# Kernel tuning notes

Measured on AMD Instinct MI355X. Metric: run time of the kernel, lower is better.

## Reference

```python
import jax, jax.numpy as jnp
import numpy as np

B, H, W = 8, 64, 64
DIM_RGB, DIM_PL, EMBED, OUT = 256, 256, 128, 256
BN_EPS = 1e-5


def conv1x1(x, w, b=None):
    # x: (B,C,H,W), w: (D,C) -> (B,D,H,W)
    y = jnp.einsum('bchw,dc->bdhw', x, w)
    if b is not None:
        y = y + b[None, :, None, None]
    return y


def spatial_attention(q, k, v, scale):
    # q,k,v: (B,D,H,W)
    b, d, h, w = q.shape
    n = h * w
    qf = q.reshape(b, d, n).transpose(0, 2, 1)   # (B,N,D)
    kf = k.reshape(b, d, n)                       # (B,D,N)
    vf = v.reshape(b, d, n).transpose(0, 2, 1)   # (B,N,D)
    attn = jax.nn.softmax(jnp.einsum('bnd,bdm->bnm', qf, kf) * scale, axis=-1)
    out = jnp.einsum('bnm,bmd->bnd', attn, vf)   # (B,N,D)
    return out.transpose(0, 2, 1).reshape(b, d, h, w)


def setup_inputs() -> dict:
    key = jax.random.key(0)
    ks = jax.random.split(key, 20)
    s = 0.05
    inp = {
        'f_rgb': jax.random.normal(ks[0], (B, DIM_RGB, H, W), jnp.float32),
        'f_pl': jax.random.normal(ks[1], (B, DIM_PL, H, W), jnp.float32),
        'w_q_rgb': jax.random.normal(ks[2], (EMBED, DIM_RGB), jnp.float32) * s,
        'b_q_rgb': jax.random.normal(ks[3], (EMBED,), jnp.float32) * s,
        'w_k_pl': jax.random.normal(ks[4], (EMBED, DIM_PL), jnp.float32) * s,
        'b_k_pl': jax.random.normal(ks[5], (EMBED,), jnp.float32) * s,
        'w_v_pl': jax.random.normal(ks[6], (EMBED, DIM_PL), jnp.float32) * s,
        'b_v_pl': jax.random.normal(ks[7], (EMBED,), jnp.float32) * s,
        'w_q_pl': jax.random.normal(ks[8], (EMBED, DIM_PL), jnp.float32) * s,
        'b_q_pl': jax.random.normal(ks[9], (EMBED,), jnp.float32) * s,
        'w_k_rgb': jax.random.normal(ks[10], (EMBED, DIM_RGB), jnp.float32) * s,
        'b_k_rgb': jax.random.normal(ks[11], (EMBED,), jnp.float32) * s,
        'w_v_rgb': jax.random.normal(ks[12], (EMBED, DIM_RGB), jnp.float32) * s,
        'b_v_rgb': jax.random.normal(ks[13], (EMBED,), jnp.float32) * s,
        'w_proj': jax.random.normal(ks[14], (OUT, 2 * EMBED), jnp.float32) * s,
        'bn_gamma': jnp.ones((OUT,), jnp.float32),
        'bn_beta': jnp.zeros((OUT,), jnp.float32),
        'bn_mean': jax.random.normal(ks[15], (OUT,), jnp.float32) * 0.01,
        'bn_var': jax.random.uniform(ks[16], (OUT,), jnp.float32, 0.5, 1.5),
    }
    return inp


def reference(f_rgb, f_pl, w_q_rgb, b_q_rgb, w_k_pl, b_k_pl, w_v_pl, b_v_pl,
              w_q_pl, b_q_pl, w_k_rgb, b_k_rgb, w_v_rgb, b_v_rgb,
              w_proj, bn_gamma, bn_beta, bn_mean, bn_var):
    scale = EMBED ** -0.5
    out_rgb2pl = spatial_attention(
        conv1x1(f_rgb, w_q_rgb, b_q_rgb),
        conv1x1(f_pl, w_k_pl, b_k_pl),
        conv1x1(f_pl, w_v_pl, b_v_pl), scale)
    out_pl2rgb = spatial_attention(
        conv1x1(f_pl, w_q_pl, b_q_pl),
        conv1x1(f_rgb, w_k_rgb, b_k_rgb),
        conv1x1(f_rgb, w_v_rgb, b_v_rgb), scale)
    combined = jnp.concatenate([out_rgb2pl, out_pl2rgb], axis=1)  # (B,2E,H,W)
    y = conv1x1(combined, w_proj)  # no bias
    # BatchNorm2d (inference form) + ReLU
    inv = bn_gamma * jax.lax.rsqrt(bn_var + BN_EPS)
    y = y * inv[None, :, None, None] + (bn_beta - bn_mean * inv)[None, :, None, None]
    return jax.nn.relu(y)
```

## Files before the change

### kernel.cpp

```cpp
#include <hip/hip_runtime.h>
#include <hip/hip_bf16.h>
#include <hip/hip_fp16.h>

typedef _Float16 f16;
typedef _Float16 f16x8 __attribute__((ext_vector_type(8)));
typedef _Float16 f16x4 __attribute__((ext_vector_type(4)));
typedef float f32x4 __attribute__((ext_vector_type(4)));

#define NP   4096
#define NB   8
#define CINC 256
#define EMB  128
#define OUTC 256
#define BN_EPS 1e-5f

#define DSZ  ((size_t)NB * NP * EMB)
#define TSZ  (2 * DSZ)

__global__ __launch_bounds__(256) void proj_all_kernel(
    const float* __restrict__ Xrgb, const float* __restrict__ Xpl,
    const float* __restrict__ w0, const float* __restrict__ b0,
    const float* __restrict__ w1, const float* __restrict__ b1,
    const float* __restrict__ w2, const float* __restrict__ b2,
    const float* __restrict__ w3, const float* __restrict__ b3,
    const float* __restrict__ w4, const float* __restrict__ b4,
    const float* __restrict__ w5, const float* __restrict__ b5,
    f16* __restrict__ Qt, f16* __restrict__ Kt, f16* __restrict__ Vn)
{
    const int m0 = blockIdx.x * 128;
    const int p  = blockIdx.y;
    const int b  = blockIdx.z;
    const int s  = (p >= 3) ? 1 : 0;
    const int j  = p - s * 3;
    const int tid = threadIdx.x;
    const int w = tid >> 6, lane = tid & 63, quad = lane >> 4, lr = lane & 15;

    const float* X  = s ? Xpl : Xrgb;
    const float* W  = p == 0 ? w0 : p == 1 ? w1 : p == 2 ? w2
                    : p == 3 ? w3 : p == 4 ? w4 : w5;
    const float* Bi = p == 0 ? b0 : p == 1 ? b1 : p == 2 ? b2
                    : p == 3 ? b3 : p == 4 ? b4 : b5;

    __shared__ __align__(16) f16 smem[128 * 72 * 2];
    f16* Al = smem;
    f16* Bl = smem + 128 * 72;

    f32x4 acc[2][8];
    #pragma unroll
    for (int mi = 0; mi < 2; ++mi)
        #pragma unroll
        for (int ni = 0; ni < 8; ++ni) acc[mi][ni] = (f32x4){0.f, 0.f, 0.f, 0.f};

    for (int kt = 0; kt < 4; ++kt) {
        const int kc0 = kt * 64;
        __syncthreads();
        for (int s2 = tid; s2 < 1024; s2 += 256) {
            const int n = s2 & 127, cg = s2 >> 7;
            f16 tmp[8];
            #pragma unroll
            for (int jj = 0; jj < 8; ++jj)
                tmp[jj] = (f16)X[((size_t)b * CINC + kc0 + cg * 8 + jj) * NP + m0 + n];
            *(f16x8*)&Al[n * 72 + cg * 8] = *(const f16x8*)tmp;
        }
        for (int s2 = tid; s2 < 1024; s2 += 256) {
            const int d = s2 >> 3, cg = s2 & 7;
            f16 tmp[8];
            #pragma unroll
            for (int jj = 0; jj < 8; ++jj)
                tmp[jj] = (f16)W[(size_t)d * CINC + kc0 + cg * 8 + jj];
            *(f16x8*)&Bl[d * 72 + cg * 8] = *(const f16x8*)tmp;
        }
        __syncthreads();
        #pragma unroll
        for (int ks = 0; ks < 2; ++ks) {
            f16x8 af[2], bfr[8];
            #pragma unroll
            for (int mi = 0; mi < 2; ++mi)
                af[mi] = *(const f16x8*)&Al[(w * 32 + mi * 16 + lr) * 72 + ks * 32 + quad * 8];
            #pragma unroll
            for (int ni = 0; ni < 8; ++ni)
                bfr[ni] = *(const f16x8*)&Bl[(ni * 16 + lr) * 72 + ks * 32 + quad * 8];
            #pragma unroll
            for (int mi = 0; mi < 2; ++mi)
                #pragma unroll
                for (int ni = 0; ni < 8; ++ni)
                    acc[mi][ni] = __builtin_amdgcn_mfma_f32_16x16x32_f16(
                        af[mi], bfr[ni], acc[mi][ni], 0, 0, 0);
        }
    }

    float bias[8];
    #pragma unroll
    for (int ni = 0; ni < 8; ++ni) bias[ni] = Bi[ni * 16 + lr];

    if (j < 2) {
        f16* out = (j == 0) ? (Qt + (size_t)s * DSZ) : (Kt + (size_t)(1 - s) * DSZ);
        #pragma unroll
        for (int mi = 0; mi < 2; ++mi)
            #pragma unroll
            for (int ni = 0; ni < 8; ++ni)
                #pragma unroll
                for (int r = 0; r < 4; ++r) {
                    const int n = m0 + w * 32 + mi * 16 + quad * 4 + r;
                    out[((size_t)b * NP + n) * EMB + ni * 16 + lr] =
                        (f16)(acc[mi][ni][r] + bias[ni]);
                }
    } else {
        f16* outV = Vn + (size_t)(1 - s) * DSZ;
        __syncthreads();
        f16* T = smem;
        #pragma unroll
        for (int mi = 0; mi < 2; ++mi)
            #pragma unroll
            for (int ni = 0; ni < 8; ++ni)
                #pragma unroll
                for (int r = 0; r < 4; ++r)
                    T[(ni * 16 + lr) * 136 + w * 32 + mi * 16 + quad * 4 + r] =
                        (f16)(acc[mi][ni][r] + bias[ni]);
        __syncthreads();
        for (int s2 = tid; s2 < 2048; s2 += 256) {
            const int d = s2 >> 4, n8 = (s2 & 15) * 8;
            *(f16x8*)&outV[((size_t)b * EMB + d) * NP + m0 + n8] =
                *(const f16x8*)&T[d * 136 + n8];
        }
    }
}

__global__ __launch_bounds__(256, 2) void attn_kernel(
    const f16* __restrict__ Qt, const f16* __restrict__ Kt,
    const f16* __restrict__ Vn, f16* __restrict__ combT)
{
    const int bid = blockIdx.x;
    const int g = bid & 15, dir = g >> 3, b = g & 7;
    const int n0 = (bid >> 4) * 128;
    const int tid = threadIdx.x;
    const int w = tid >> 6, lane = tid & 63, quad = lane >> 4, lr = lane & 15;

    const f16* Q = Qt + ((size_t)dir * NB + b) * NP * EMB;
    const f16* K = Kt + ((size_t)dir * NB + b) * NP * EMB;
    const f16* V = Vn + ((size_t)dir * NB + b) * (size_t)EMB * NP;

    __shared__ __align__(16) f16 Kl[64][136];
    __shared__ __align__(16) f16 Vl[128][72];

    const int qbase = n0 + w * 32;

    f16x8 qf[2][4];
    #pragma unroll
    for (int nt = 0; nt < 2; ++nt)
        #pragma unroll
        for (int cc = 0; cc < 4; ++cc) {
            f16x8 q = *(const f16x8*)&Q[(size_t)(qbase + nt * 16 + lr) * EMB + cc * 32 + quad * 8];
            #pragma unroll
            for (int k = 0; k < 8; ++k)
                q[k] = q[k] * (f16)0.12752749f;
            qf[nt][cc] = q;
        }

    f32x4 O[2][8];
    #pragma unroll
    for (int nt = 0; nt < 2; ++nt)
        #pragma unroll
        for (int dt = 0; dt < 8; ++dt) O[nt][dt] = (f32x4){0.f, 0.f, 0.f, 0.f};
    float rs[2] = {0.f, 0.f};

    for (int m0 = 0; m0 < NP; m0 += 64) {
        __syncthreads();
        #pragma unroll
        for (int i = 0; i < 4; ++i) {
            const int s2 = i * 256 + tid;
            const int mm = s2 >> 4, dc = s2 & 15;
            *(f16x8*)&Kl[mm][dc * 8] = *(const f16x8*)&K[(size_t)(m0 + mm) * EMB + dc * 8];
        }
        #pragma unroll
        for (int i = 0; i < 4; ++i) {
            const int s2 = i * 256 + tid;
            const int d = s2 >> 3, mc = s2 & 7;
            *(f16x8*)&Vl[d][mc * 8] = *(const f16x8*)&V[(size_t)d * NP + m0 + mc * 8];
        }
        __syncthreads();

        #pragma unroll
        for (int ms = 0; ms < 4; ++ms) {
            f16x8 kf[4];
            #pragma unroll
            for (int cc = 0; cc < 4; ++cc)
                kf[cc] = *(const f16x8*)&Kl[ms * 16 + lr][cc * 32 + quad * 8];

            f16x4 ppk[2];
            #pragma unroll
            for (int nt = 0; nt < 2; ++nt) {
                f32x4 sa = (f32x4){0.f, 0.f, 0.f, 0.f};
                #pragma unroll
                for (int cc = 0; cc < 4; ++cc)
                    sa = __builtin_amdgcn_mfma_f32_16x16x32_f16(kf[cc], qf[nt][cc], sa, 0, 0, 0);
                const float e0 = __builtin_amdgcn_exp2f(sa[0]);
                const float e1 = __builtin_amdgcn_exp2f(sa[1]);
                const float e2 = __builtin_amdgcn_exp2f(sa[2]);
                const float e3 = __builtin_amdgcn_exp2f(sa[3]);
                rs[nt] += (e0 + e1) + (e2 + e3);
                f16x4 pp;
                pp[0] = (f16)e0; pp[1] = (f16)e1; pp[2] = (f16)e2; pp[3] = (f16)e3;
                ppk[nt] = pp;
            }

            #pragma unroll
            for (int dt = 0; dt < 8; ++dt) {
                const f16x4 vf = *(const f16x4*)&Vl[dt * 16 + lr][ms * 16 + quad * 4];
                O[0][dt] = __builtin_amdgcn_mfma_f32_16x16x16f16(ppk[0], vf, O[0][dt], 0, 0, 0);
                O[1][dt] = __builtin_amdgcn_mfma_f32_16x16x16f16(ppk[1], vf, O[1][dt], 0, 0, 0);
            }
        }
    }

    #pragma unroll
    for (int nt = 0; nt < 2; ++nt) {
        rs[nt] += __shfl_xor(rs[nt], 16);
        rs[nt] += __shfl_xor(rs[nt], 32);
    }
    #pragma unroll
    for (int nt = 0; nt < 2; ++nt) {
        float iv[4];
        #pragma unroll
        for (int r = 0; r < 4; ++r)
            iv[r] = 1.0f / __shfl(rs[nt], quad * 4 + r, 64);
        #pragma unroll
        for (int dt = 0; dt < 8; ++dt)
            #pragma unroll
            for (int r = 0; r < 4; ++r) {
                const int n = qbase + nt * 16 + quad * 4 + r;
                combT[((size_t)b * NP + n) * OUTC + dir * EMB + dt * 16 + lr] =
                    (f16)(O[nt][dt][r] * iv[r]);
            }
    }
}

__global__ __launch_bounds__(256) void proj_out_kernel(
    const f16* __restrict__ combT, const float* __restrict__ Wp,
    const float* __restrict__ G, const float* __restrict__ Be,
    const float* __restrict__ Mu, const float* __restrict__ Va,
    float* __restrict__ out)
{
    const int m0 = blockIdx.x * 128;
    const int o0 = blockIdx.y * 128;
    const int b  = blockIdx.z;
    const int tid = threadIdx.x;
    const int w = tid >> 6, lane = tid & 63, quad = lane >> 4, lr = lane & 15;

    __shared__ __align__(16) f16 smem[128 * 72 * 2];
    f16* Al = smem;
    f16* Bl = smem + 128 * 72;

    f32x4 acc[2][8];
    #pragma unroll
    for (int mi = 0; mi < 2; ++mi)
        #pragma unroll
        for (int ni = 0; ni < 8; ++ni) acc[mi][ni] = (f32x4){0.f, 0.f, 0.f, 0.f};

    for (int kt = 0; kt < 4; ++kt) {
        const int kc0 = kt * 64;
        __syncthreads();
        #pragma unroll
        for (int i = 0; i < 4; ++i) {
            const int s2 = i * 256 + tid;
            const int n = s2 >> 3, cg = s2 & 7;
            *(f16x8*)&Al[n * 72 + cg * 8] =
                *(const f16x8*)&combT[((size_t)b * NP + m0 + n) * OUTC + kc0 + cg * 8];
        }
        for (int s2 = tid; s2 < 1024; s2 += 256) {
            const int d = s2 >> 3, cg = s2 & 7;
            f16 tmp[8];
            #pragma unroll
            for (int jj = 0; jj < 8; ++jj)
                tmp[jj] = (f16)Wp[(size_t)(o0 + d) * OUTC + kc0 + cg * 8 + jj];
            *(f16x8*)&Bl[d * 72 + cg * 8] = *(const f16x8*)tmp;
        }
        __syncthreads();
        #pragma unroll
        for (int ks = 0; ks < 2; ++ks) {
            f16x8 af[2], bfr[8];
            #pragma unroll
            for (int mi = 0; mi < 2; ++mi)
                af[mi] = *(const f16x8*)&Al[(w * 32 + mi * 16 + lr) * 72 + ks * 32 + quad * 8];
            #pragma unroll
            for (int ni = 0; ni < 8; ++ni)
                bfr[ni] = *(const f16x8*)&Bl[(ni * 16 + lr) * 72 + ks * 32 + quad * 8];
            #pragma unroll
            for (int mi = 0; mi < 2; ++mi)
                #pragma unroll
                for (int ni = 0; ni < 8; ++ni)
                    acc[mi][ni] = __builtin_amdgcn_mfma_f32_16x16x32_f16(
                        af[mi], bfr[ni], acc[mi][ni], 0, 0, 0);
        }
    }

    __syncthreads();
    f16* T = smem;
    #pragma unroll
    for (int ni = 0; ni < 8; ++ni) {
        const int o = o0 + ni * 16 + lr;
        const float iv = G[o] * rsqrtf(Va[o] + BN_EPS);
        const float sh = Be[o] - Mu[o] * iv;
        #pragma unroll
        for (int mi = 0; mi < 2; ++mi)
            #pragma unroll
            for (int r = 0; r < 4; ++r)
                T[(ni * 16 + lr) * 136 + w * 32 + mi * 16 + quad * 4 + r] =
                    (f16)fmaxf(acc[mi][ni][r] * iv + sh, 0.f);
    }
    __syncthreads();
    for (int s2 = tid; s2 < 2048; s2 += 256) {
        const int o = s2 >> 4, n8 = (s2 & 15) * 8;
        const f16x8 v = *(const f16x8*)&T[o * 136 + n8];
        const size_t off = ((size_t)b * OUTC + o0 + o) * NP + m0 + n8;
        #pragma unroll
        for (int k = 0; k < 8; ++k) out[off + k] = (float)v[k];
    }
}

extern "C" void kernel_launch(void* const* d_in, const int* in_sizes, int n_in,
                              void* d_out, int out_size, void* d_ws, size_t ws_size,
                              hipStream_t stream) {
    const float* f_rgb   = (const float*)d_in[0];
    const float* f_pl    = (const float*)d_in[1];
    const float* w_q_rgb = (const float*)d_in[2];  const float* b_q_rgb = (const float*)d_in[3];
    const float* w_k_pl  = (const float*)d_in[4];  const float* b_k_pl  = (const float*)d_in[5];
    const float* w_v_pl  = (const float*)d_in[6];  const float* b_v_pl  = (const float*)d_in[7];
    const float* w_q_pl  = (const float*)d_in[8];  const float* b_q_pl  = (const float*)d_in[9];
    const float* w_k_rgb = (const float*)d_in[10]; const float* b_k_rgb = (const float*)d_in[11];
    const float* w_v_rgb = (const float*)d_in[12]; const float* b_v_rgb = (const float*)d_in[13];
    const float* w_proj  = (const float*)d_in[14];
    const float* bn_g    = (const float*)d_in[15]; const float* bn_b = (const float*)d_in[16];
    const float* bn_m    = (const float*)d_in[17]; const float* bn_v = (const float*)d_in[18];

    f16* Qt    = (f16*)d_ws;
    f16* Kt    = Qt + TSZ;
    f16* Vn    = Kt + TSZ;
    f16* combT = Vn + TSZ;

    proj_all_kernel<<<dim3(32, 6, 8), 256, 0, stream>>>(
        f_rgb, f_pl,
        w_q_rgb, b_q_rgb, w_k_rgb, b_k_rgb, w_v_rgb, b_v_rgb,
        w_q_pl,  b_q_pl,  w_k_pl,  b_k_pl,  w_v_pl,  b_v_pl,
        Qt, Kt, Vn);

    attn_kernel<<<512, 256, 0, stream>>>(Qt, Kt, Vn, combT);

    proj_out_kernel<<<dim3(32, 2, 8), 256, 0, stream>>>(
        combT, w_proj, bn_g, bn_b, bn_m, bn_v, (float*)d_out);
}
```

Before: 357.8 us.

## Rewrite attention with 32x32 MFMA, larger query tiles, swizzled LDS, double buffering

The attention kernel moves from 16x16 MFMA tiles to 32x32x16 MFMA, with each wave owning 64 queries (256 per block, half the blocks). The K and V tiles are double-buffered in LDS with register staging, so the next tile's global loads overlap the current compute. An XOR swizzle replaces the padded layout to avoid bank conflicts, and P is repacked between lane halves with shuffles. The aim is more reuse per LDS load and hidden memory latency, at the cost of more registers, occupancy 1, and only 256 blocks.

New measurement: 372.6 us. 1.04x slower.

```diff
diff --git a/kernel.cpp b/kernel.cpp
--- a/kernel.cpp
+++ b/kernel.cpp
@@ -6,6 +6,7 @@
 typedef _Float16 f16x8 __attribute__((ext_vector_type(8)));
 typedef _Float16 f16x4 __attribute__((ext_vector_type(4)));
 typedef float f32x4 __attribute__((ext_vector_type(4)));
+typedef float f32x16 __attribute__((ext_vector_type(16)));
 
 #define NP   4096
 #define NB   8
@@ -126,111 +127,166 @@
     }
 }
 
-__global__ __launch_bounds__(256, 2) void attn_kernel(
+__device__ __forceinline__ unsigned pkf16(float a, float b) {
+    union { f16 h[2]; unsigned u; } t;
+    t.h[0] = (f16)a; t.h[1] = (f16)b;
+    return t.u;
+}
+
+__global__ __launch_bounds__(256, 1) void attn_kernel(
     const f16* __restrict__ Qt, const f16* __restrict__ Kt,
     const f16* __restrict__ Vn, f16* __restrict__ combT)
 {
     const int bid = blockIdx.x;
     const int g = bid & 15, dir = g >> 3, b = g & 7;
-    const int n0 = (bid >> 4) * 128;
+    const int n0 = (bid >> 4) * 256;
     const int tid = threadIdx.x;
-    const int w = tid >> 6, lane = tid & 63, quad = lane >> 4, lr = lane & 15;
-
-    const f16* Q = Qt + ((size_t)dir * NB + b) * NP * EMB;
-    const f16* K = Kt + ((size_t)dir * NB + b) * NP * EMB;
-    const f16* V = Vn + ((size_t)dir * NB + b) * (size_t)EMB * NP;
-
-    __shared__ __align__(16) f16 Kl[64][136];
-    __shared__ __align__(16) f16 Vl[128][72];
-
-    const int qbase = n0 + w * 32;
-
-    f16x8 qf[2][4];
-    #pragma unroll
-    for (int nt = 0; nt < 2; ++nt)
-        #pragma unroll
-        for (int cc = 0; cc < 4; ++cc) {
-            f16x8 q = *(const f16x8*)&Q[(size_t)(qbase + nt * 16 + lr) * EMB + cc * 32 + quad * 8];
-            #pragma unroll
-            for (int k = 0; k < 8; ++k)
-                q[k] = q[k] * (f16)0.12752749f;
-            qf[nt][cc] = q;
-        }
-
-    f32x4 O[2][8];
-    #pragma unroll
-    for (int nt = 0; nt < 2; ++nt)
-        #pragma unroll
-        for (int dt = 0; dt < 8; ++dt) O[nt][dt] = (f32x4){0.f, 0.f, 0.f, 0.f};
+    const int w = tid >> 6, lane = tid & 63;
+    const int l31 = lane & 31, hi = lane >> 5;
+
+    const f16* __restrict__ Q = Qt + ((size_t)dir * NB + b) * NP * EMB;
+    const f16* __restrict__ K = Kt + ((size_t)dir * NB + b) * NP * EMB;
+    const f16* __restrict__ V = Vn + ((size_t)dir * NB + b) * (size_t)EMB * NP;
+
+    __shared__ __align__(16) f16 Kl[2][64 * 128];
+    __shared__ __align__(16) f16 Vl[2][128 * 64];
+
+    const int qbase = n0 + w * 64;
+
+    f16x8 qf[2][8];
+    #pragma unroll
+    for (int q32 = 0; q32 < 2; ++q32)
+        #pragma unroll
+        for (int d16 = 0; d16 < 8; ++d16) {
+            f16x8 q = *(const f16x8*)&Q[(size_t)(qbase + q32 * 32 + l31) * EMB + d16 * 16 + hi * 8];
+            #pragma unroll
+            for (int jj = 0; jj < 8; ++jj)
+                q[jj] = q[jj] * (f16)0.12752749f;
+            qf[q32][d16] = q;
+        }
+
+    f32x16 O[4][2];
+    #pragma unroll
+    for (int d32 = 0; d32 < 4; ++d32)
+        #pragma unroll
+        for (int q32 = 0; q32 < 2; ++q32) O[d32][q32] = (f32x16)(0.0f);
     float rs[2] = {0.f, 0.f};
 
-    for (int m0 = 0; m0 < NP; m0 += 64) {
-        __syncthreads();
+    const int krp = lane >> 4, kp = lane & 15;
+    const int vrp = lane >> 3, vp = lane & 7;
+    f16x8 stK[4], stV[4];
+
+    auto stage_load = [&](int m0) {
         #pragma unroll
         for (int i = 0; i < 4; ++i) {
-            const int s2 = i * 256 + tid;
-            const int mm = s2 >> 4, dc = s2 & 15;
-            *(f16x8*)&Kl[mm][dc * 8] = *(const f16x8*)&K[(size_t)(m0 + mm) * EMB + dc * 8];
+            const int r = w * 16 + i * 4 + krp;
+            const int c = kp ^ (r & 7);
+            stK[i] = *(const f16x8*)&K[(size_t)(m0 + r) * EMB + c * 8];
         }
         #pragma unroll
         for (int i = 0; i < 4; ++i) {
-            const int s2 = i * 256 + tid;
-            const int d = s2 >> 3, mc = s2 & 7;
-            *(f16x8*)&Vl[d][mc * 8] = *(const f16x8*)&V[(size_t)d * NP + m0 + mc * 8];
-        }
-        __syncthreads();
-
-        #pragma unroll
-        for (int ms = 0; ms < 4; ++ms) {
-            f16x8 kf[4];
-            #pragma unroll
-            for (int cc = 0; cc < 4; ++cc)
-                kf[cc] = *(const f16x8*)&Kl[ms * 16 + lr][cc * 32 + quad * 8];
-
-            f16x4 ppk[2];
-            #pragma unroll
-            for (int nt = 0; nt < 2; ++nt) {
-                f32x4 sa = (f32x4){0.f, 0.f, 0.f, 0.f};
-                #pragma unroll
-                for (int cc = 0; cc < 4; ++cc)
-                    sa = __builtin_amdgcn_mfma_f32_16x16x32_f16(kf[cc], qf[nt][cc], sa, 0, 0, 0);
-                const float e0 = __builtin_amdgcn_exp2f(sa[0]);
-                const float e1 = __builtin_amdgcn_exp2f(sa[1]);
-                const float e2 = __builtin_amdgcn_exp2f(sa[2]);
-                const float e3 = __builtin_amdgcn_exp2f(sa[3]);
-                rs[nt] += (e0 + e1) + (e2 + e3);
-                f16x4 pp;
-                pp[0] = (f16)e0; pp[1] = (f16)e1; pp[2] = (f16)e2; pp[3] = (f16)e3;
-                ppk[nt] = pp;
+            const int r = w * 32 + i * 8 + vrp;
+            const int c = vp ^ (r & 7);
+            stV[i] = *(const f16x8*)&V[(size_t)r * NP + m0 + c * 8];
+        }
+    };
+    auto stage_write = [&](int buf) {
+        #pragma unroll
+        for (int i = 0; i < 4; ++i) {
+            const int r = w * 16 + i * 4 + krp;
+            *(f16x8*)&Kl[buf][r * 128 + kp * 8] = stK[i];
+        }
+        #pragma unroll
+        for (int i = 0; i < 4; ++i) {
+            const int r = w * 32 + i * 8 + vrp;
+            *(f16x8*)&Vl[buf][r * 64 + vp * 8] = stV[i];
+        }
+    };
+
+    stage_load(0);
+    stage_write(0);
+    int cur = 0;
+
+    for (int t = 0; t < NP / 64; ++t) {
+        __syncthreads();
+        if (t < NP / 64 - 1) stage_load((t + 1) * 64);
+
+        const f16* Kb = &Kl[cur][0];
+        const f16* Vb = &Vl[cur][0];
+
+        #pragma unroll
+        for (int k32 = 0; k32 < 2; ++k32) {
+            f32x16 s0 = (f32x16)(0.0f), s1 = (f32x16)(0.0f);
+            #pragma unroll
+            for (int d16 = 0; d16 < 8; ++d16) {
+                const int r = k32 * 32 + l31;
+                const int c = (d16 * 2 + hi) ^ (r & 7);
+                const f16x8 kf = *(const f16x8*)&Kb[r * 128 + c * 8];
+                s0 = __builtin_amdgcn_mfma_f32_32x32x16_f16(kf, qf[0][d16], s0, 0, 0, 0);
+                s1 = __builtin_amdgcn_mfma_f32_32x32x16_f16(kf, qf[1][d16], s1, 0, 0, 0);
             }
 
-            #pragma unroll
-            for (int dt = 0; dt < 8; ++dt) {
-                const f16x4 vf = *(const f16x4*)&Vl[dt * 16 + lr][ms * 16 + quad * 4];
-                O[0][dt] = __builtin_amdgcn_mfma_f32_16x16x16f16(ppk[0], vf, O[0][dt], 0, 0, 0);
-                O[1][dt] = __builtin_amdgcn_mfma_f32_16x16x16f16(ppk[1], vf, O[1][dt], 0, 0, 0);
+            f16x8 pb[2][2];
+            #pragma unroll
+            for (int q32 = 0; q32 < 2; ++q32) {
+                const f32x16 s = q32 ? s1 : s0;
+                float e[16];
+                #pragma unroll
+                for (int i = 0; i < 16; ++i) e[i] = __builtin_amdgcn_exp2f(s[i]);
+                float sum = 0.f;
+                #pragma unroll
+                for (int i = 0; i < 16; ++i) sum += e[i];
+                rs[q32] += sum;
+                #pragma unroll
+                for (int g2 = 0; g2 < 2; ++g2) {
+                    const unsigned pa  = pkf16(e[g2 * 8 + 0], e[g2 * 8 + 1]);
+                    const unsigned pbu = pkf16(e[g2 * 8 + 2], e[g2 * 8 + 3]);
+                    const unsigned pc  = pkf16(e[g2 * 8 + 4], e[g2 * 8 + 5]);
+                    const unsigned pd  = pkf16(e[g2 * 8 + 6], e[g2 * 8 + 7]);
+                    const unsigned recv0 = __shfl_xor(hi ? pa : pc, 32);
+                    const unsigned recv1 = __shfl_xor(hi ? pbu : pd, 32);
+                    union { unsigned u[4]; f16x8 v; } pu;
+                    pu.u[0] = hi ? recv0 : pa;
+                    pu.u[1] = hi ? recv1 : pbu;
+                    pu.u[2] = hi ? pc : recv0;
+                    pu.u[3] = hi ? pd : recv1;
+                    pb[g2][q32] = pu.v;
+                }
             }
-        }
-    }
-
-    #pragma unroll
-    for (int nt = 0; nt < 2; ++nt) {
-        rs[nt] += __shfl_xor(rs[nt], 16);
-        rs[nt] += __shfl_xor(rs[nt], 32);
-    }
-    #pragma unroll
-    for (int nt = 0; nt < 2; ++nt) {
-        float iv[4];
-        #pragma unroll
-        for (int r = 0; r < 4; ++r)
-            iv[r] = 1.0f / __shfl(rs[nt], quad * 4 + r, 64);
-        #pragma unroll
-        for (int dt = 0; dt < 8; ++dt)
-            #pragma unroll
-            for (int r = 0; r < 4; ++r) {
-                const int n = qbase + nt * 16 + quad * 4 + r;
-                combT[((size_t)b * NP + n) * OUTC + dir * EMB + dt * 16 + lr] =
-                    (f16)(O[nt][dt][r] * iv[r]);
+
+            #pragma unroll
+            for (int g2 = 0; g2 < 2; ++g2) {
+                #pragma unroll
+                for (int d32 = 0; d32 < 4; ++d32) {
+                    const int r = d32 * 32 + l31;
+                    const int c = ((k32 * 2 + g2) * 2 + hi) ^ (r & 7);
+                    const f16x8 vf = *(const f16x8*)&Vb[r * 64 + c * 8];
+                    O[d32][0] = __builtin_amdgcn_mfma_f32_32x32x16_f16(vf, pb[g2][0], O[d32][0], 0, 0, 0);
+                    O[d32][1] = __builtin_amdgcn_mfma_f32_32x32x16_f16(vf, pb[g2][1], O[d32][1], 0, 0, 0);
+                }
+            }
+        }
+
+        if (t < NP / 64 - 1) stage_write(cur ^ 1);
+        cur ^= 1;
+    }
+
+    rs[0] += __shfl_xor(rs[0], 32);
+    rs[1] += __shfl_xor(rs[1], 32);
+    const float inv[2] = {1.0f / rs[0], 1.0f / rs[1]};
+    #pragma unroll
+    for (int q32 = 0; q32 < 2; ++q32) {
+        const int n = qbase + q32 * 32 + l31;
+        #pragma unroll
+        for (int d32 = 0; d32 < 4; ++d32)
+            #pragma unroll
+            for (int tq = 0; tq < 4; ++tq) {
+                f16 o4[4];
+                #pragma unroll
+                for (int jj = 0; jj < 4; ++jj)
+                    o4[jj] = (f16)(O[d32][q32][tq * 4 + jj] * inv[q32]);
+                *(f16x4*)&combT[((size_t)b * NP + n) * OUTC + dir * EMB + d32 * 32 + tq * 8 + hi * 4] =
+                    *(const f16x4*)o4;
             }
     }
 }
@@ -344,7 +400,7 @@
         w_q_pl,  b_q_pl,  w_k_pl,  b_k_pl,  w_v_pl,  b_v_pl,
         Qt, Kt, Vn);
 
-    attn_kernel<<<512, 256, 0, stream>>>(Qt, Kt, Vn, combT);
+    attn_kernel<<<256, 256, 0, stream>>>(Qt, Kt, Vn, combT);
 
     proj_out_kernel<<<dim3(32, 2, 8), 256, 0, stream>>>(
         combT, w_proj, bn_g, bn_b, bn_m, bn_v, (float*)d_out);
```
